# Performance work log

Hardware: AMD Instinct MI355X
Metric: run time of the kernel (lower is better)

Reference implementation:

```python
import jax, jax.numpy as jnp
import numpy as np
import math

B, S, D_MODEL = 2, 2048, 1024
H = 16
DK = D_MODEL // H          # 64, down-proj per-stream dim
NOPE, ROPE = 128, 64
D_HEAD = NOPE + ROPE       # 192 = d_latent // H
D_LATENT = H * D_HEAD      # 3072
ROT_DIM = 2 * ((ROPE // 2) // 2)  # rotary dim actually rotated = qk_rope_dim//2 = 32
EPS = 1e-6


def _rmsnorm(x, w):
    out = x * jax.lax.rsqrt(jnp.mean(x * x, axis=-1, keepdims=True) + EPS)
    return out * w


def _apply_rope(x):
    # x: [b, h, s, d]; rotate first ROT_DIM channels, interleaved pairing
    s = x.shape[-2]
    inv_freq = 1.0 / (10000.0 ** (jnp.arange(0, ROT_DIM, 2, dtype=jnp.float32) / ROT_DIM))
    freqs = jnp.arange(s, dtype=jnp.float32)[:, None] * inv_freq[None, :]  # [s, ROT_DIM//2]
    freqs = jnp.repeat(freqs, 2, axis=-1)  # [s, ROT_DIM], (f0,f0,f1,f1,...)
    cos, sin = jnp.cos(freqs), jnp.sin(freqs)
    xl, xr = x[..., :ROT_DIM], x[..., ROT_DIM:]
    x1, x2 = xl[..., 0::2], xl[..., 1::2]
    rot = jnp.stack([-x2, x1], axis=-1).reshape(xl.shape)
    xl = xl * cos + rot * sin
    return jnp.concatenate([xl, xr], axis=-1)


def setup_inputs() -> dict:
    key = jax.random.key(0)
    ks = jax.random.split(key, 5)
    sc = 0.02
    x = jax.random.normal(ks[0], (B, S, D_MODEL), jnp.float32)
    mask = jnp.broadcast_to(jnp.tril(jnp.ones((S, S), jnp.int32)), (B, S, S))
    w_down = jax.random.normal(ks[1], (D_MODEL, 3 * DK), jnp.float32) * sc
    rms_w = jnp.ones((3 * DK,), jnp.float32)
    w_up = jax.random.normal(ks[2], (3 * DK, 3 * D_LATENT), jnp.float32) * sc
    w_o = jax.random.normal(ks[3], (D_LATENT, D_MODEL), jnp.float32) * sc
    return {"x": x, "mask": mask, "w_down": w_down, "rms_w": rms_w, "w_up": w_up, "w_o": w_o}


def reference(x, mask, w_down, rms_w, w_up, w_o):
    h = x @ w_down                        # [b, s, 3*dk]
    h = _rmsnorm(h, rms_w)
    qkv = h @ w_up                        # [b, s, 3*d_latent]
    q, k, v = jnp.split(qkv, 3, axis=-1)  # each [b, s, d_latent]

    def to_heads(t):
        # einops '(d h)': d outer, h inner
        return t.reshape(B, S, D_HEAD, H).transpose(0, 3, 1, 2)  # [b, h, s, d]

    q, k, v = to_heads(q), to_heads(k), to_heads(v)
    q_nope, q_rope = q[..., :NOPE], q[..., NOPE:]
    k_nope, k_rope = k[..., :NOPE], k[..., NOPE:]
    q_rope = _apply_rope(q_rope)
    k_rope = _apply_rope(k_rope)

    scores = (jnp.einsum('bhid,bhjd->bhij', q_nope, k_nope)
              + jnp.einsum('bhid,bhjd->bhij', q_rope, k_rope))
    scores = scores / math.sqrt(NOPE + ROPE)
    scores = jnp.where(mask[:, None] == 0, -1e9, scores)
    attn = jax.nn.softmax(scores, axis=-1)

    out = jnp.einsum('bhij,bhjd->bhid', attn, v)        # [b, h, s, d]
    out = out.transpose(0, 2, 1, 3).reshape(B, S, D_LATENT)  # 'b h s d -> b s (h d)'
    return out @ w_o
```

## Files before the change

### kernel.cpp

```cpp
#include <hip/hip_runtime.h>
#include <stdint.h>
#include <stddef.h>


typedef __bf16 bf16x8 __attribute__((ext_vector_type(8)));
typedef float  f32x4  __attribute__((ext_vector_type(4)));

#define MFMA16x16(a,b,c) __builtin_amdgcn_mfma_f32_16x16x32_bf16((a),(b),(c),0,0,0)

__device__ __forceinline__ uint16_t f2bf(float f){
  union { float f; uint32_t u; } v; v.f = f;
  uint32_t u = v.u + 0x7fffu + ((v.u >> 16) & 1u);
  return (uint16_t)(u >> 16);
}
__device__ __forceinline__ bf16x8 load_frag(const uint16_t* p){
  uint4 u = *reinterpret_cast<const uint4*>(p);
  return __builtin_bit_cast(bf16x8, u);
}
__device__ __forceinline__ f32x4 fzero(){
  f32x4 z = {0.f, 0.f, 0.f, 0.f};
  return z;
}
__device__ __forceinline__ uint32_t pack2(float a, float b){
  return (uint32_t)f2bf(a) | ((uint32_t)f2bf(b) << 16);
}
__device__ __forceinline__ void gl2lds16(const uint16_t* g, uint16_t* l){
  __builtin_amdgcn_global_load_lds(
      (const __attribute__((address_space(1))) uint32_t*)g,
      (__attribute__((address_space(3))) uint32_t*)l,
      16, 0, 0);
}

__global__ __launch_bounds__(256) void k_transpose_cvt(const float* __restrict__ in,
                                                       uint16_t* __restrict__ out,
                                                       int R, int C){
  __shared__ float t[32][33];
  const int tc = blockIdx.x * 32;
  const int tr = blockIdx.y * 32;
  const int j = threadIdx.x & 31, i0 = threadIdx.x >> 5;
  for(int ii = 0; ii < 4; ++ii){
    int r = i0 + ii * 8;
    t[r][j] = in[(size_t)(tr + r) * C + tc + j];
  }
  __syncthreads();
  for(int ii = 0; ii < 4; ++ii){
    int c = i0 + ii * 8;
    out[(size_t)(tc + c) * R + tr + j] = f2bf(t[j][c]);
  }
}

__global__ __launch_bounds__(256) void k_down_mfma(const float* __restrict__ x,
                                                   const uint16_t* __restrict__ wdt,
                                                   const float* __restrict__ rms_w,
                                                   uint16_t* __restrict__ h_out){
  __shared__ __align__(16) uint16_t as[32 * 64];
  __shared__ float hsq[32];
  const int tid  = threadIdx.x;
  const int wave = tid >> 6, lane = tid & 63;
  const int ml = lane & 15, qd = lane >> 4;
  const int m0 = blockIdx.x * 32;
  const int n0w = wave * 48;
  if(tid < 32) hsq[tid] = 0.f;

  f32x4 acc[2][3];
#pragma unroll
  for(int mt = 0; mt < 2; ++mt)
#pragma unroll
    for(int nt = 0; nt < 3; ++nt) acc[mt][nt] = fzero();

  const int srow = tid >> 3, sc = tid & 7;
  for(int kt = 0; kt < 16; ++kt){
    const float* src = x + (size_t)(m0 + srow) * 1024 + kt * 64 + sc * 8;
    float4 a = *reinterpret_cast<const float4*>(src);
    float4 b = *reinterpret_cast<const float4*>(src + 4);
    uint4 pk;
    pk.x = pack2(a.x, a.y); pk.y = pack2(a.z, a.w);
    pk.z = pack2(b.x, b.y); pk.w = pack2(b.z, b.w);
    __syncthreads();
    *reinterpret_cast<uint4*>(as + srow * 64 + ((sc ^ (srow & 7)) * 8)) = pk;
    __syncthreads();
#pragma unroll
    for(int kk = 0; kk < 2; ++kk){
      bf16x8 af[2];
#pragma unroll
      for(int mt = 0; mt < 2; ++mt){
        int row = mt * 16 + ml;
        af[mt] = load_frag(as + row * 64 + (((kk * 4 + qd) ^ (row & 7)) * 8));
      }
#pragma unroll
      for(int nt = 0; nt < 3; ++nt){
        bf16x8 bfr = load_frag(wdt + (size_t)(n0w + nt * 16 + ml) * 1024 + kt * 64 + kk * 32 + qd * 8);
#pragma unroll
        for(int mt = 0; mt < 2; ++mt)
          acc[mt][nt] = MFMA16x16(af[mt], bfr, acc[mt][nt]);
      }
    }
  }
  __syncthreads();
#pragma unroll
  for(int mt = 0; mt < 2; ++mt)
#pragma unroll
    for(int r = 0; r < 4; ++r){
      float s = acc[mt][0][r]*acc[mt][0][r] + acc[mt][1][r]*acc[mt][1][r] + acc[mt][2][r]*acc[mt][2][r];
#pragma unroll
      for(int off = 1; off < 16; off <<= 1) s += __shfl_xor(s, off);
      if(ml == 0) atomicAdd(&hsq[mt * 16 + qd * 4 + r], s);
    }
  __syncthreads();
  float rw[3];
#pragma unroll
  for(int nt = 0; nt < 3; ++nt) rw[nt] = rms_w[n0w + nt * 16 + ml];
#pragma unroll
  for(int mt = 0; mt < 2; ++mt)
#pragma unroll
    for(int r = 0; r < 4; ++r){
      int row = mt * 16 + qd * 4 + r;
      float scl = rsqrtf(hsq[row] * (1.0f / 192.0f) + 1e-6f);
#pragma unroll
      for(int nt = 0; nt < 3; ++nt)
        h_out[(size_t)(m0 + row) * 192 + n0w + nt * 16 + ml] = f2bf(acc[mt][nt][r] * scl * rw[nt]);
    }
}

__global__ __launch_bounds__(256) void k_gemm_up(const uint16_t* __restrict__ hmat,
                                                 const uint16_t* __restrict__ wt,
                                                 uint16_t* __restrict__ q_t,
                                                 uint16_t* __restrict__ k_t,
                                                 uint16_t* __restrict__ v_t){
  __shared__ __align__(16) uint16_t rp[16 * 129 * 8];
  const int wave = threadIdx.x >> 6, lane = threadIdx.x & 63;
  const int ml = lane & 15, qd = lane >> 4;
  const int m0 = blockIdx.y * 32;
  const int bx = blockIdx.x;
  const int which = bx / 6;
  const int d0b = (bx % 6) * 32;
  const int n0w = bx * 512 + wave * 128;
  const int d0w = d0b + wave * 8;

  bf16x8 af[2][6];
#pragma unroll
  for(int mt = 0; mt < 2; ++mt)
#pragma unroll
    for(int kk = 0; kk < 6; ++kk)
      af[mt][kk] = load_frag(hmat + (size_t)(m0 + mt * 16 + ml) * 192 + kk * 32 + qd * 8);

  f32x4 acc[8][2];
#pragma unroll
  for(int nt = 0; nt < 8; ++nt){ acc[nt][0] = fzero(); acc[nt][1] = fzero(); }
#pragma unroll
  for(int nt = 0; nt < 8; ++nt){
#pragma unroll
    for(int kk = 0; kk < 6; ++kk){
      bf16x8 b = load_frag(wt + (size_t)(n0w + nt * 16 + ml) * 192 + kk * 32 + qd * 8);
      acc[nt][0] = MFMA16x16(af[0][kk], b, acc[nt][0]);
      acc[nt][1] = MFMA16x16(af[1][kk], b, acc[nt][1]);
    }
  }

  const int b   = m0 >> 11;
  const int s0  = m0 & 2047;
  const int kt2 = s0 >> 6;
  const int row0 = s0 & 63;
  uint4* rp4 = (uint4*)rp;

  if(which < 2){
    const float qs = which ? 1.0f : 0.07216878364870322f;
    const bool rope = (d0w >= 128) && (d0w < 160);
#pragma unroll
    for(int mt = 0; mt < 2; ++mt)
#pragma unroll
      for(int r = 0; r < 4; ++r){
        int t = mt * 16 + qd * 4 + r;
        int s = s0 + t;
        float v[8];
#pragma unroll
        for(int nt = 0; nt < 8; ++nt) v[nt] = acc[nt][mt][r] * qs;
        if(rope){
#pragma unroll
          for(int pi = 0; pi < 4; ++pi){
            int fi = (d0w + 2 * pi - 128) >> 1;
            float invf = __expf(-(float)fi * 0.5756462732485114f);
            float sn, cs;
            sincosf((float)s * invf, &sn, &cs);
            float e = v[2 * pi], o = v[2 * pi + 1];
            v[2 * pi]     = e * cs - o * sn;
            v[2 * pi + 1] = o * cs + e * sn;
          }
        }
        uint4 pk;
        pk.x = pack2(v[0], v[1]); pk.y = pack2(v[2], v[3]);
        pk.z = pack2(v[4], v[5]); pk.w = pack2(v[6], v[7]);
        rp4[ml * 129 + t * 4 + (wave ^ (t & 3))] = pk;
      }
  } else {
#pragma unroll
    for(int nt = 0; nt < 8; ++nt){
      int dl = wave * 8 + nt;
#pragma unroll
      for(int mt = 0; mt < 2; ++mt){
        int jc = mt * 2 + (qd >> 1);
        int slot = ml * 129 + dl * 4 + (jc ^ (dl & 3));
        uint2 pk;
        pk.x = pack2(acc[nt][mt][0], acc[nt][mt][1]);
        pk.y = pack2(acc[nt][mt][2], acc[nt][mt][3]);
        *(reinterpret_cast<uint2*>(rp + slot * 8) + (qd & 1)) = pk;
      }
    }
  }
  __syncthreads();

  if(which < 2){
    uint16_t* dst = which ? k_t : q_t;
    const int cb = d0b >> 3;
#pragma unroll
    for(int it = 0; it < 8; ++it){
      int h = wave * 4 + (it & 3), rhalf = it >> 2;
      int tloc = rhalf * 16 + (lane >> 2), p = lane & 3;
      int row = row0 + tloc;
      uint4 val = rp4[h * 129 + tloc * 4 + p];
      size_t off = ((size_t)(b * 16 + h) * 32 + kt2) * 12288
                 + (size_t)row * 192 + ((cb ^ (tloc & 4)) + p) * 8;
      *reinterpret_cast<uint4*>(dst + off) = val;
    }
  } else {
    const int cs0 = row0 >> 3;
#pragma unroll
    for(int it = 0; it < 8; ++it){
      int h = wave * 4 + (it & 3), dhalf = it >> 2;
      int dl = dhalf * 16 + (lane >> 2), p = lane & 3;
      uint4 val = rp4[h * 129 + dl * 4 + p];
      size_t off = ((size_t)(b * 16 + h) * 32 + kt2) * 12288
                 + (size_t)(d0b + dl) * 64 + ((cs0 ^ (dl & 4)) + p) * 8;
      *reinterpret_cast<uint4*>(v_t + off) = val;
    }
  }
}

__global__ __launch_bounds__(256, 2) void k_attn(const uint16_t* __restrict__ q_t,
                                                 const uint16_t* __restrict__ k_t,
                                                 const uint16_t* __restrict__ v_t,
                                                 uint16_t* __restrict__ attn_out){
  __shared__ __align__(16) uint16_t smem[30720];
  const int tid  = threadIdx.x;
  const int wave = tid >> 6;
  const int lane = tid & 63;
  const int ml   = lane & 15;
  const int qd   = lane >> 4;
  const int bx   = blockIdx.x;
  const int bh   = bx & 31;
  const int qb   = (bx < 256) ? (15 - (bx >> 5)) : ((bx >> 5) - 8);
  const int last = 4 * qb + 3;

  uint16_t* const kb0 = smem;
  uint16_t* const kb1 = smem + 6144;
  uint16_t* const vb0 = smem + 12288;
  uint16_t* const vb1 = smem + 18944;
  uint16_t* const psw = smem + 25600 + wave * 1280;

  const uint16_t* kbase = k_t + (size_t)bh * 393216;
  const uint16_t* vbase = v_t + (size_t)bh * 393216;
  const int hh = bh & 15, bb = bh >> 4;

  const int c_  = (lane & 3) ^ ((lane >> 3) & 3);
  const int s7_ = (lane >> 2) & 7;
  const int vg_ = (lane >> 2) * 64;
  const int voff0 = vg_ + ((c_ ^ s7_) * 8);
  const int voff1 = vg_ + (((4 + c_) ^ s7_) * 8);
  const int vpo = ml * 32 + ((qd ^ ((ml >> 1) & 3)) * 8);

  bf16x8 qf[2][6];
  {
    const int row = wave * 16 + ml;
    const int sw = row & 7;
#pragma unroll
    for(int t = 0; t < 2; ++t){
      const uint16_t* qtb = q_t + ((size_t)bh * 32 + qb * 2 + t) * 12288 + (size_t)row * 192;
#pragma unroll
      for(int kk = 0; kk < 6; ++kk)
        qf[t][kk] = load_frag(qtb + (((kk * 4 + qd) ^ sw) * 8));
    }
  }
  __builtin_amdgcn_sched_barrier(0);
  asm volatile("s_waitcnt vmcnt(0)" ::: "memory");
  __builtin_amdgcn_sched_barrier(0);

  ((uint32_t*)(vb0 + 6144))[tid] = 0x3F803F80u;
  ((uint32_t*)(vb1 + 6144))[tid] = 0x3F803F80u;

  auto stageKV = [&](int kt, int sel){
    const uint16_t* ksrc = kbase + (size_t)(kt >> 1) * 12288 + (kt & 1) * 6144
                         + wave * 1536 + lane * 8;
    uint16_t* kd = (sel ? kb1 : kb0) + wave * 1536;
    gl2lds16(ksrc,        kd);
    gl2lds16(ksrc + 512,  kd + 512);
    gl2lds16(ksrc + 1024, kd + 1024);
    const int vo = (kt & 1) ? voff1 : voff0;
    const uint16_t* vsrc = vbase + (size_t)(kt >> 1) * 12288 + (size_t)(wave * 3) * 1024 + vo;
    uint16_t* vd = (sel ? vb1 : vb0) + wave * 1536;
    gl2lds16(vsrc,        vd);
    gl2lds16(vsrc + 1024, vd + 512);
    gl2lds16(vsrc + 2048, vd + 1024);
  };

  stageKV(0, 0);
  asm volatile("s_waitcnt lgkmcnt(0)" ::: "memory");

  f32x4 o[2][13];
#pragma unroll
  for(int t = 0; t < 2; ++t)
#pragma unroll
    for(int i = 0; i < 13; ++i) o[t][i] = fzero();

  const int r0 = qb * 128 + wave * 16;
  const int r1 = r0 + 64;
  int cur = 0;
  for(int kt = 0; kt <= last; ++kt){
    if(kt < last){
      stageKV(kt + 1, cur ^ 1);
      __builtin_amdgcn_sched_barrier(0);
      asm volatile("s_waitcnt vmcnt(6)" ::: "memory");
      __builtin_amdgcn_sched_barrier(0);
    } else {
      asm volatile("s_waitcnt vmcnt(0)" ::: "memory");
      __builtin_amdgcn_sched_barrier(0);
    }
    __builtin_amdgcn_s_barrier();

    const int kl = kt * 32;
    if(kl <= r1 + 15){
      const uint16_t* kc = cur ? kb1 : kb0;
      const uint16_t* vc = cur ? vb1 : vb0;
      const bool a0 = (kl <= r0 + 15);

      f32x4 s[2][2];
      s[0][0] = fzero(); s[0][1] = fzero(); s[1][0] = fzero(); s[1][1] = fzero();
      __builtin_amdgcn_s_setprio(1);
#pragma unroll
      for(int nt = 0; nt < 2; ++nt){
        int row = nt * 16 + ml;
#pragma unroll
        for(int kk = 0; kk < 6; ++kk){
          bf16x8 bfr = load_frag(kc + row * 192 + (((kk * 4 + qd) ^ (row & 7)) * 8));
          if(a0) s[0][nt] = MFMA16x16(qf[0][kk], bfr, s[0][nt]);
          s[1][nt] = MFMA16x16(qf[1][kk], bfr, s[1][nt]);
        }
      }
      __builtin_amdgcn_s_setprio(0);

#pragma unroll
      for(int t = 0; t < 2; ++t){
        if(t == 0 && !a0) continue;
        const int rq = t ? r1 : r0;
        const bool diag = (kl + 31 > rq);
#pragma unroll
        for(int nt = 0; nt < 2; ++nt)
#pragma unroll
          for(int r = 0; r < 4; ++r){
            float v = s[t][nt][r];
            if(diag){
              int i = rq + qd * 4 + r;
              int j = kl + nt * 16 + ml;
              if(j > i) v = -1e9f;
            }
            psw[(t * 16 + qd * 4 + r) * 40 + nt * 16 + ml] = f2bf(__expf(v));
          }
      }
      bf16x8 pa0 = load_frag(psw + ml * 40 + qd * 8);
      bf16x8 pa1 = load_frag(psw + (16 + ml) * 40 + qd * 8);
      __builtin_amdgcn_s_setprio(1);
#pragma unroll
      for(int dt = 0; dt < 13; ++dt){
        bf16x8 vbf = load_frag(vc + dt * 512 + vpo);
        if(a0) o[0][dt] = MFMA16x16(pa0, vbf, o[0][dt]);
        o[1][dt] = MFMA16x16(pa1, vbf, o[1][dt]);
      }
      __builtin_amdgcn_s_setprio(0);
    }
    __builtin_amdgcn_s_barrier();
    cur ^= 1;
  }

#pragma unroll
  for(int t = 0; t < 2; ++t){
    const int rq = t ? r1 : r0;
#pragma unroll
    for(int r = 0; r < 4; ++r){
      int i = rq + qd * 4 + r;
      float inv = 1.0f / o[t][12][r];
      size_t obase = ((size_t)bb * 2048 + i) * 3072 + hh * 192;
#pragma unroll
      for(int dt = 0; dt < 12; ++dt)
        attn_out[obase + dt * 16 + ml] = f2bf(o[t][dt][r] * inv);
    }
  }
}

__global__ __launch_bounds__(256) void k_gemm_o_tile(const uint16_t* __restrict__ a,
                                                     const uint16_t* __restrict__ wt,
                                                     float* __restrict__ part){
  __shared__ __align__(16) uint16_t as[128 * 64];
  __shared__ __align__(16) uint16_t bs[128 * 64];
  const int wave = threadIdx.x >> 6, lane = threadIdx.x & 63;
  const int ml = lane & 15, qd = lane >> 4;
  const int m0 = blockIdx.y * 128, n0 = blockIdx.x * 128;
  const int kz = blockIdx.z;
  const int mo = (wave >> 1) * 64, no = (wave & 1) * 64;

  const int lrow = lane >> 3;
  const int gch  = (lane & 7) ^ (lrow & 7);
  const uint16_t* abase = a  + (size_t)(m0 + lrow) * 3072 + kz * 1536 + gch * 8;
  const uint16_t* bbase = wt + (size_t)(n0 + lrow) * 3072 + kz * 1536 + gch * 8;

  f32x4 acc[4][4];
#pragma unroll
  for(int mt = 0; mt < 4; ++mt)
#pragma unroll
    for(int nt = 0; nt < 4; ++nt) acc[mt][nt] = fzero();

  for(int kt = 0; kt < 24; ++kt){
    __syncthreads();
#pragma unroll
    for(int it = 0; it < 4; ++it){
      int seg = it * 4 + wave;
      gl2lds16(abase + (size_t)seg * 24576 + kt * 64, as + seg * 512);
      gl2lds16(bbase + (size_t)seg * 24576 + kt * 64, bs + seg * 512);
    }
    __syncthreads();
#pragma unroll
    for(int ks2 = 0; ks2 < 2; ++ks2){
      bf16x8 af[4], bfr[4];
#pragma unroll
      for(int mt = 0; mt < 4; ++mt){
        int row = mo + mt * 16 + ml;
        af[mt] = load_frag(as + row * 64 + (((ks2 * 4 + qd) ^ (row & 7)) * 8));
      }
#pragma unroll
      for(int nt = 0; nt < 4; ++nt){
        int row = no + nt * 16 + ml;
        bfr[nt] = load_frag(bs + row * 64 + (((ks2 * 4 + qd) ^ (row & 7)) * 8));
      }
#pragma unroll
      for(int mt = 0; mt < 4; ++mt)
#pragma unroll
        for(int nt = 0; nt < 4; ++nt)
          acc[mt][nt] = MFMA16x16(af[mt], bfr[nt], acc[mt][nt]);
    }
  }

  float* dst = part + (size_t)kz * 4096 * 1024;
#pragma unroll
  for(int mt = 0; mt < 4; ++mt)
#pragma unroll
    for(int nt = 0; nt < 4; ++nt)
#pragma unroll
      for(int r = 0; r < 4; ++r){
        int row = m0 + mo + mt * 16 + qd * 4 + r;
        int col = n0 + no + nt * 16 + ml;
        dst[(size_t)row * 1024 + col] = acc[mt][nt][r];
      }
}

__global__ __launch_bounds__(256) void k_addout(const float* __restrict__ part,
                                                float* __restrict__ out){
  int i = blockIdx.x * 256 + threadIdx.x;
  const float4* p0 = (const float4*)part;
  const float4* p1 = p0 + (size_t)1048576;
  float4 a = p0[i], b = p1[i];
  float4 c; c.x = a.x + b.x; c.y = a.y + b.y; c.z = a.z + b.z; c.w = a.w + b.w;
  ((float4*)out)[i] = c;
}


extern "C" void kernel_launch(void* const* d_in, const int* in_sizes, int n_in,
                              void* d_out, int out_size, void* d_ws, size_t ws_size,
                              hipStream_t stream) {
  (void)in_sizes; (void)n_in; (void)out_size; (void)ws_size;
  const float* x      = (const float*)d_in[0];
  const float* w_down = (const float*)d_in[2];
  const float* rms_w  = (const float*)d_in[3];
  const float* w_up   = (const float*)d_in[4];
  const float* w_o    = (const float*)d_in[5];
  float* out = (float*)d_out;

  char* ws = (char*)d_ws;
  uint16_t* h_bf   = (uint16_t*)(ws);
  uint16_t* w_up_t = (uint16_t*)(ws + 1572864);
  uint16_t* w_o_t  = (uint16_t*)(ws + 5111808);
  uint16_t* w_dn_t = (uint16_t*)(ws + 11403264);
  uint16_t* q_tb   = (uint16_t*)(ws + 11796480);
  uint16_t* k_tb   = (uint16_t*)(ws + 36962304);
  uint16_t* v_tb   = (uint16_t*)(ws + 62128128);
  uint16_t* attnO  = (uint16_t*)(ws + 87293952);
  float*    part   = (float*)(ws + 11796480);

  k_transpose_cvt<<<dim3(288, 6), 256, 0, stream>>>(w_up, w_up_t, 192, 9216);
  k_transpose_cvt<<<dim3(32, 96), 256, 0, stream>>>(w_o,  w_o_t,  3072, 1024);
  k_transpose_cvt<<<dim3(6, 32),  256, 0, stream>>>(w_down, w_dn_t, 1024, 192);
  k_down_mfma<<<128, 256, 0, stream>>>(x, w_dn_t, rms_w, h_bf);
  k_gemm_up<<<dim3(18, 128), 256, 0, stream>>>(h_bf, w_up_t, q_tb, k_tb, v_tb);
  k_attn<<<512, 256, 0, stream>>>(q_tb, k_tb, v_tb, attnO);
  k_gemm_o_tile<<<dim3(8, 32, 2), 256, 0, stream>>>(attnO, w_o_t, part);
  k_addout<<<4096, 256, 0, stream>>>(part, out);
}
```

Before: 375.1 us.

## Split attention KV range across two wave halves with shared-memory reduction

Each attention block now runs 8 waves. The causal KV range for a 128-row query tile is split in two, with each group of 4 waves streaming half of the key/value tiles through its own double buffer. The partial output accumulators, including the row-sum column, are then summed through shared memory before normalization and store. This is meant to shorten the long serial KV loop per block and balance causal work, because the grid now processes each query block once instead of pairing tiles. The cost is double the LDS use, an extra reduction pass, and possible occupancy pressure from the 512-thread blocks.

```diff
diff --git a/kernel.cpp b/kernel.cpp
--- a/kernel.cpp
+++ b/kernel.cpp
@@ -236,26 +236,24 @@
   }
 }
 
-__global__ __launch_bounds__(256, 2) void k_attn(const uint16_t* __restrict__ q_t,
+__global__ __launch_bounds__(512, 2) void k_attn(const uint16_t* __restrict__ q_t,
                                                  const uint16_t* __restrict__ k_t,
                                                  const uint16_t* __restrict__ v_t,
                                                  uint16_t* __restrict__ attn_out){
-  __shared__ __align__(16) uint16_t smem[30720];
+  __shared__ __align__(16) uint16_t smem[61440];
   const int tid  = threadIdx.x;
   const int wave = tid >> 6;
   const int lane = tid & 63;
   const int ml   = lane & 15;
   const int qd   = lane >> 4;
+  const int hw   = wave & 3;
+  const int half = wave >> 2;
   const int bx   = blockIdx.x;
   const int bh   = bx & 31;
-  const int qb   = (bx < 256) ? (15 - (bx >> 5)) : ((bx >> 5) - 8);
-  const int last = 4 * qb + 3;
-
-  uint16_t* const kb0 = smem;
-  uint16_t* const kb1 = smem + 6144;
-  uint16_t* const vb0 = smem + 12288;
-  uint16_t* const vb1 = smem + 18944;
-  uint16_t* const psw = smem + 25600 + wave * 1280;
+  const int s    = 15 - (bx >> 5);
+  const int Lh   = 2 * s + 2;
+
+  uint16_t* const psw = smem + 51200 + wave * 1280;
 
   const uint16_t* kbase = k_t + (size_t)bh * 393216;
   const uint16_t* vbase = v_t + (size_t)bh * 393216;
@@ -270,40 +268,46 @@
 
   bf16x8 qf[2][6];
   {
-    const int row = wave * 16 + ml;
-    const int sw = row & 7;
+    const uint16_t* qtb = q_t + ((size_t)bh * 32 + 2 * s + (hw >> 1)) * 12288;
 #pragma unroll
     for(int t = 0; t < 2; ++t){
-      const uint16_t* qtb = q_t + ((size_t)bh * 32 + qb * 2 + t) * 12288 + (size_t)row * 192;
+      int row = (hw & 1) * 32 + t * 16 + ml;
+      const uint16_t* qr = qtb + (size_t)row * 192;
+      int sw = row & 7;
 #pragma unroll
       for(int kk = 0; kk < 6; ++kk)
-        qf[t][kk] = load_frag(qtb + (((kk * 4 + qd) ^ sw) * 8));
-    }
-  }
-  __builtin_amdgcn_sched_barrier(0);
-  asm volatile("s_waitcnt vmcnt(0)" ::: "memory");
-  __builtin_amdgcn_sched_barrier(0);
-
-  ((uint32_t*)(vb0 + 6144))[tid] = 0x3F803F80u;
-  ((uint32_t*)(vb1 + 6144))[tid] = 0x3F803F80u;
+        qf[t][kk] = load_frag(qr + (((kk * 4 + qd) ^ sw) * 8));
+    }
+  }
+
+  {
+    uint32_t* o01 = (uint32_t*)(smem + 24576 + (tid >> 8) * 6656 + 6144);
+    uint32_t* o23 = (uint32_t*)(smem + 24576 + (2 + (tid >> 8)) * 6656 + 6144);
+    o01[tid & 255] = 0x3F803F80u;
+    o23[tid & 255] = 0x3F803F80u;
+  }
+  asm volatile("s_waitcnt lgkmcnt(0)" ::: "memory");
 
   auto stageKV = [&](int kt, int sel){
-    const uint16_t* ksrc = kbase + (size_t)(kt >> 1) * 12288 + (kt & 1) * 6144
-                         + wave * 1536 + lane * 8;
-    uint16_t* kd = (sel ? kb1 : kb0) + wave * 1536;
-    gl2lds16(ksrc,        kd);
-    gl2lds16(ksrc + 512,  kd + 512);
-    gl2lds16(ksrc + 1024, kd + 1024);
+    const int b4 = half * 2 + sel;
+#pragma unroll
+    for(int it = 0; it < 3; ++it){
+      int seg = hw * 3 + it;
+      const uint16_t* ksrc = kbase + (size_t)(kt >> 1) * 12288 + (kt & 1) * 6144
+                           + seg * 512 + lane * 8;
+      gl2lds16(ksrc, smem + b4 * 6144 + seg * 512);
+    }
     const int vo = (kt & 1) ? voff1 : voff0;
-    const uint16_t* vsrc = vbase + (size_t)(kt >> 1) * 12288 + (size_t)(wave * 3) * 1024 + vo;
-    uint16_t* vd = (sel ? vb1 : vb0) + wave * 1536;
-    gl2lds16(vsrc,        vd);
-    gl2lds16(vsrc + 1024, vd + 512);
-    gl2lds16(vsrc + 2048, vd + 1024);
+#pragma unroll
+    for(int it = 0; it < 3; ++it){
+      int seg = hw * 3 + it;
+      const uint16_t* vsrc = vbase + (size_t)(kt >> 1) * 12288 + (size_t)seg * 1024 + vo;
+      gl2lds16(vsrc, smem + 24576 + b4 * 6656 + seg * 512);
+    }
   };
 
-  stageKV(0, 0);
-  asm volatile("s_waitcnt lgkmcnt(0)" ::: "memory");
+  const int kt0 = half * Lh;
+  stageKV(kt0, 0);
 
   f32x4 o[2][13];
 #pragma unroll
@@ -311,12 +315,12 @@
 #pragma unroll
     for(int i = 0; i < 13; ++i) o[t][i] = fzero();
 
-  const int r0 = qb * 128 + wave * 16;
-  const int r1 = r0 + 64;
+  const int r0 = s * 128 + hw * 32;
+  const int r1 = r0 + 16;
   int cur = 0;
-  for(int kt = 0; kt <= last; ++kt){
-    if(kt < last){
-      stageKV(kt + 1, cur ^ 1);
+  for(int i = 0; i < Lh; ++i){
+    if(i + 1 < Lh){
+      stageKV(kt0 + i + 1, cur ^ 1);
       __builtin_amdgcn_sched_barrier(0);
       asm volatile("s_waitcnt vmcnt(6)" ::: "memory");
       __builtin_amdgcn_sched_barrier(0);
@@ -326,14 +330,14 @@
     }
     __builtin_amdgcn_s_barrier();
 
-    const int kl = kt * 32;
+    const int kl = (kt0 + i) * 32;
     if(kl <= r1 + 15){
-      const uint16_t* kc = cur ? kb1 : kb0;
-      const uint16_t* vc = cur ? vb1 : vb0;
+      const uint16_t* kc = smem + (half * 2 + cur) * 6144;
+      const uint16_t* vc = smem + 24576 + (half * 2 + cur) * 6656;
       const bool a0 = (kl <= r0 + 15);
 
-      f32x4 s[2][2];
-      s[0][0] = fzero(); s[0][1] = fzero(); s[1][0] = fzero(); s[1][1] = fzero();
+      f32x4 sv[2][2];
+      sv[0][0] = fzero(); sv[0][1] = fzero(); sv[1][0] = fzero(); sv[1][1] = fzero();
       __builtin_amdgcn_s_setprio(1);
 #pragma unroll
       for(int nt = 0; nt < 2; ++nt){
@@ -341,8 +345,8 @@
 #pragma unroll
         for(int kk = 0; kk < 6; ++kk){
           bf16x8 bfr = load_frag(kc + row * 192 + (((kk * 4 + qd) ^ (row & 7)) * 8));
-          if(a0) s[0][nt] = MFMA16x16(qf[0][kk], bfr, s[0][nt]);
-          s[1][nt] = MFMA16x16(qf[1][kk], bfr, s[1][nt]);
+          if(a0) sv[0][nt] = MFMA16x16(qf[0][kk], bfr, sv[0][nt]);
+          sv[1][nt] = MFMA16x16(qf[1][kk], bfr, sv[1][nt]);
         }
       }
       __builtin_amdgcn_s_setprio(0);
@@ -350,17 +354,17 @@
 #pragma unroll
       for(int t = 0; t < 2; ++t){
         if(t == 0 && !a0) continue;
-        const int rq = t ? r1 : r0;
+        const int rq = r0 + t * 16;
         const bool diag = (kl + 31 > rq);
 #pragma unroll
         for(int nt = 0; nt < 2; ++nt)
 #pragma unroll
           for(int r = 0; r < 4; ++r){
-            float v = s[t][nt][r];
+            float v = sv[t][nt][r];
             if(diag){
-              int i = rq + qd * 4 + r;
+              int i2 = rq + qd * 4 + r;
               int j = kl + nt * 16 + ml;
-              if(j > i) v = -1e9f;
+              if(j > i2) v = -1e9f;
             }
             psw[(t * 16 + qd * 4 + r) * 40 + nt * 16 + ml] = f2bf(__expf(v));
           }
@@ -380,17 +384,31 @@
     cur ^= 1;
   }
 
-#pragma unroll
-  for(int t = 0; t < 2; ++t){
-    const int rq = t ? r1 : r0;
-#pragma unroll
-    for(int r = 0; r < 4; ++r){
-      int i = rq + qd * 4 + r;
-      float inv = 1.0f / o[t][12][r];
-      size_t obase = ((size_t)bb * 2048 + i) * 3072 + hh * 192;
-#pragma unroll
-      for(int dt = 0; dt < 12; ++dt)
-        attn_out[obase + dt * 16 + ml] = f2bf(o[t][dt][r] * inv);
+  f32x4* red = (f32x4*)smem;
+  if(half == 1){
+#pragma unroll
+    for(int t = 0; t < 2; ++t)
+#pragma unroll
+      for(int dt = 0; dt < 13; ++dt)
+        red[(hw * 2 + t) * 832 + lane * 13 + dt] = o[t][dt];
+  }
+  __syncthreads();
+  if(half == 0){
+#pragma unroll
+    for(int t = 0; t < 2; ++t){
+#pragma unroll
+      for(int dt = 0; dt < 13; ++dt)
+        o[t][dt] += red[(hw * 2 + t) * 832 + lane * 13 + dt];
+      const int rq = r0 + t * 16;
+#pragma unroll
+      for(int r = 0; r < 4; ++r){
+        int i2 = rq + qd * 4 + r;
+        float inv = 1.0f / o[t][12][r];
+        size_t obase = ((size_t)bb * 2048 + i2) * 3072 + hh * 192;
+#pragma unroll
+        for(int dt = 0; dt < 12; ++dt)
+          attn_out[obase + dt * 16 + ml] = f2bf(o[t][dt][r] * inv);
+      }
     }
   }
 }
@@ -498,7 +516,7 @@
   k_transpose_cvt<<<dim3(6, 32),  256, 0, stream>>>(w_down, w_dn_t, 1024, 192);
   k_down_mfma<<<128, 256, 0, stream>>>(x, w_dn_t, rms_w, h_bf);
   k_gemm_up<<<dim3(18, 128), 256, 0, stream>>>(h_bf, w_up_t, q_tb, k_tb, v_tb);
-  k_attn<<<512, 256, 0, stream>>>(q_tb, k_tb, v_tb, attnO);
+  k_attn<<<512, 512, 0, stream>>>(q_tb, k_tb, v_tb, attnO);
   k_gemm_o_tile<<<dim3(8, 32, 2), 256, 0, stream>>>(attnO, w_o_t, part);
   k_addout<<<4096, 256, 0, stream>>>(part, out);
 }
```

Result: faster. 342.9 us (-8.6%).
